# Kernel tuning notes

Hardware: AMD Instinct MI355X
Metric: run time of the kernel (lower is better)

## Reference

```python
import jax, jax.numpy as jnp
import numpy as np

S, B, H = 2048, 2, 2048
NP = 16            # num attention heads
HN = H // NP       # head dim = 128


def setup_inputs() -> dict:
    key = jax.random.key(0)
    k0, k1, k2 = jax.random.split(key, 3)
    hidden_states = jax.random.normal(k0, (S, B, H), dtype=jnp.float32) * 0.02
    w_qkv = jax.random.normal(k1, (3 * H, H), dtype=jnp.float32) * 0.02
    b_qkv = jnp.zeros((3 * H,), dtype=jnp.float32)
    w_dense = jax.random.normal(k2, (H, H), dtype=jnp.float32) * 0.02
    b_dense = jnp.zeros((H,), dtype=jnp.float32)
    # causal mask: True means "mask out" (strictly upper triangular)
    attention_mask = jnp.triu(jnp.ones((S, S), dtype=bool), k=1)[None, None]  # [1,1,S,S]
    return {
        "hidden_states": hidden_states,
        "attention_mask": attention_mask,
        "w_qkv": w_qkv,
        "b_qkv": b_qkv,
        "w_dense": w_dense,
        "b_dense": b_dense,
    }


def reference(hidden_states, attention_mask, w_qkv, b_qkv, w_dense, b_dense):
    s, b, h = hidden_states.shape
    # fused QKV projection (ColumnParallelLinear: y = x @ W^T + b)
    mixed = hidden_states @ w_qkv.T + b_qkv                 # [s,b,3h]
    mixed = mixed.reshape(s, b, NP, 3 * HN)
    q, k, v = jnp.split(mixed, 3, axis=-1)                  # each [s,b,np,hn]
    norm = 1.0 / jnp.sqrt(jnp.asarray(HN, hidden_states.dtype))
    # scaled QK^T -> [b,np,sq,sk]
    scores = jnp.einsum("sbnh,tbnh->bnst", q, k) * norm
    # attention_mask_func: masked_fill(mask, -10000.0)
    scores = jnp.where(attention_mask, jnp.asarray(-10000.0, scores.dtype), scores)
    # softmax in fp32 (softmax_in_fp32)
    probs = jax.nn.softmax(scores.astype(jnp.float32), axis=-1).astype(scores.dtype)
    # AV matmul -> [s,b,np,hn] -> [s,b,h]
    context = jnp.einsum("bnst,tbnh->sbnh", probs, v).reshape(s, b, h)
    # output projection (RowParallelLinear)
    out = context @ w_dense.T + b_dense
    return out
```

## Files before the change

### kernel.cpp

```cpp
#include <hip/hip_runtime.h>
#include <hip/hip_bf16.h>
#include <cstdint>
#include <cstddef>

#define SS   2048
#define BB   2
#define HH   2048
#define NHEAD 16
#define HDIM 128
#define H3   6144
#define MROWS 4096

typedef __attribute__((ext_vector_type(4))) float f32x4;
typedef __attribute__((ext_vector_type(8))) __bf16 bf16x8;
typedef __attribute__((ext_vector_type(8))) unsigned short us8;
typedef __attribute__((ext_vector_type(4))) unsigned short us4;

__device__ __forceinline__ unsigned short f2b(float f) {
    union { float f; unsigned u; } v; v.f = f;
    unsigned r = v.u + 0x7fffu + ((v.u >> 16) & 1u);
    return (unsigned short)(r >> 16);
}

__device__ __forceinline__ bf16x8 ld_b16x8(const unsigned short* p) {
    us8 u = *(const us8*)p;
    return __builtin_bit_cast(bf16x8, u);
}

__device__ __forceinline__ bf16x8 ld8_off(const unsigned short* base, int byteoff) {
    return __builtin_bit_cast(bf16x8, *(const us8*)((const char*)base + byteoff));
}

__device__ __forceinline__ int sw256(int b) { return b ^ (((b >> 8) & 7) << 4); }
__device__ __forceinline__ int sw128(int b) { return b ^ (((b >> 7) & 7) << 4); }

__device__ __forceinline__ void gload_lds16(const unsigned short* g, unsigned short* l) {
    __builtin_amdgcn_global_load_lds(
        (const __attribute__((address_space(1))) unsigned int*)g,
        (__attribute__((address_space(3))) unsigned int*)l, 16, 0, 0);
}

__global__ __launch_bounds__(256) void cvt_f32_bf16(
    const float* __restrict__ in, unsigned short* __restrict__ out, int n4)
{
    const int stride = gridDim.x * blockDim.x;
    for (int i = blockIdx.x * blockDim.x + threadIdx.x; i < n4; i += stride) {
        const float4 v = ((const float4*)in)[i];
        us4 o = { f2b(v.x), f2b(v.y), f2b(v.z), f2b(v.w) };
        ((us4*)out)[i] = o;
    }
}

__global__ __launch_bounds__(256) void transpose_v(
    const unsigned short* __restrict__ mixed,
    unsigned short* __restrict__ vt)
{
    const int st = blockIdx.x;
    const int nh = blockIdx.y;
    const int bb = blockIdx.z;
    const int tid = threadIdx.x;
    __shared__ unsigned short T[64][136];
#pragma unroll
    for (int i = 0; i < 4; ++i) {
        const int c = i * 256 + tid;
        const int sl = c >> 4, d0 = (c & 15) << 3;
        const us8 v = *(const us8*)(mixed +
            ((size_t)(st * 64 + sl) * BB + bb) * H3 + nh * 384 + 256 + d0);
        *(us8*)(&T[sl][d0]) = v;
    }
    __syncthreads();
#pragma unroll
    for (int i = 0; i < 4; ++i) {
        const int c = i * 256 + tid;
        const int d = c >> 3, sl0 = (c & 7) << 3;
        us8 o;
#pragma unroll
        for (int j = 0; j < 8; ++j) o[j] = T[sl0 + j][d];
        *(us8*)(vt + ((size_t)(bb * NHEAD + nh) * HDIM + d) * SS + st * 64 + sl0) = o;
    }
}

#define STAGE_HALF(gp, lo)                                        \
    gload_lds16((gp) + soff[0], smem + (lo) + tid * 8);           \
    gload_lds16((gp) + soff[1], smem + (lo) + 4096 + tid * 8);

template <bool F32OUT>
__global__ __launch_bounds__(512, 2) void gemm_8ph(
    const unsigned short* __restrict__ A,
    const unsigned short* __restrict__ Bw,
    const float* __restrict__ bias,
    void* __restrict__ Cout,
    int Nv, int Kv)
{
    extern __shared__ unsigned short smem[];

    const int tid  = threadIdx.x;
    const int lane = tid & 63;
    const int wave = tid >> 6;
    const int wm = wave >> 2, wn = wave & 3;
    const int bm = blockIdx.y, bn = blockIdx.x;

    const unsigned short* Ab = A  + (size_t)bm * 256 * Kv;
    const unsigned short* Bb = Bw + (size_t)bn * 256 * Kv;

    int soff[2];
#pragma unroll
    for (int i = 0; i < 2; ++i) {
        const int p = (i * 512 + tid) * 16;
        const int l = p ^ (((p >> 7) & 7) << 4);
        soff[i] = (l >> 7) * Kv + ((l & 127) >> 1);
    }

    f32x4 acc[8][4];
#pragma unroll
    for (int m = 0; m < 8; ++m)
#pragma unroll
        for (int n = 0; n < 4; ++n) acc[m][n] = (f32x4){0.f, 0.f, 0.f, 0.f};

    const int frow = lane & 15;
    const int g16  = (lane >> 4) << 4;
    const int swx  = (frow & 7) << 4;
    const int kx0  = g16 ^ swx;
    const int kx1  = (64 + g16) ^ swx;
    const int aRowB = (wm * 128 + frow) * 128;
    const int bRowB = 65536 + (wn * 64 + frow) * 128;

    const int NT = Kv >> 6;

    STAGE_HALF(Ab,                 0);
    STAGE_HALF(Ab + 128 * Kv,      8192);
    STAGE_HALF(Bb,                 32768);
    STAGE_HALF(Bb + 128 * Kv,      40960);
    STAGE_HALF(Bb + 64,            16384 + 32768);
    STAGE_HALF(Bb + 128 * Kv + 64, 16384 + 40960);
    asm volatile("s_waitcnt vmcnt(4)" ::: "memory");
    __builtin_amdgcn_s_barrier();

    for (int t = 0; t < NT; ++t) {
        const int j   = t & 1;
        const int jo  = j * 32768;
        const int joE = j * 16384;
        const int jnE = (j ^ 1) * 16384;
        const int cA  = (t + 1 < NT) ? (t + 1) * 64 : (NT - 1) * 64;
        const int cB  = (t + 2 < NT) ? (t + 2) * 64 : (NT - 1) * 64;

        bf16x8 bb[4][2];

        {
            bf16x8 a00 = ld8_off(smem, jo + aRowB + 0 * 2048 + kx0);
            bf16x8 a01 = ld8_off(smem, jo + aRowB + 0 * 2048 + kx1);
            bf16x8 a10 = ld8_off(smem, jo + aRowB + 1 * 2048 + kx0);
            bf16x8 a11 = ld8_off(smem, jo + aRowB + 1 * 2048 + kx1);
#pragma unroll
            for (int n = 0; n < 4; ++n) {
                bb[n][0] = ld8_off(smem, jo + bRowB + n * 2048 + kx0);
                bb[n][1] = ld8_off(smem, jo + bRowB + n * 2048 + kx1);
            }
            STAGE_HALF(Ab + cA, jnE);
            __builtin_amdgcn_s_barrier();
            asm volatile("s_waitcnt lgkmcnt(0)" ::: "memory");
            __builtin_amdgcn_sched_barrier(0);
            __builtin_amdgcn_s_setprio(1);
#pragma unroll
            for (int n = 0; n < 4; ++n) {
                acc[0][n] = __builtin_amdgcn_mfma_f32_16x16x32_bf16(a00, bb[n][0], acc[0][n], 0, 0, 0);
                acc[0][n] = __builtin_amdgcn_mfma_f32_16x16x32_bf16(a01, bb[n][1], acc[0][n], 0, 0, 0);
                acc[1][n] = __builtin_amdgcn_mfma_f32_16x16x32_bf16(a10, bb[n][0], acc[1][n], 0, 0, 0);
                acc[1][n] = __builtin_amdgcn_mfma_f32_16x16x32_bf16(a11, bb[n][1], acc[1][n], 0, 0, 0);
            }
            __builtin_amdgcn_s_setprio(0);
            __builtin_amdgcn_s_barrier();
        }
        {
            bf16x8 a00 = ld8_off(smem, jo + aRowB + 2 * 2048 + kx0);
            bf16x8 a01 = ld8_off(smem, jo + aRowB + 2 * 2048 + kx1);
            bf16x8 a10 = ld8_off(smem, jo + aRowB + 3 * 2048 + kx0);
            bf16x8 a11 = ld8_off(smem, jo + aRowB + 3 * 2048 + kx1);
            STAGE_HALF(Ab + 128 * Kv + cA, jnE + 8192);
            __builtin_amdgcn_s_barrier();
            asm volatile("s_waitcnt lgkmcnt(0)" ::: "memory");
            __builtin_amdgcn_sched_barrier(0);
            __builtin_amdgcn_s_setprio(1);
#pragma unroll
            for (int n = 0; n < 4; ++n) {
                acc[2][n] = __builtin_amdgcn_mfma_f32_16x16x32_bf16(a00, bb[n][0], acc[2][n], 0, 0, 0);
                acc[2][n] = __builtin_amdgcn_mfma_f32_16x16x32_bf16(a01, bb[n][1], acc[2][n], 0, 0, 0);
                acc[3][n] = __builtin_amdgcn_mfma_f32_16x16x32_bf16(a10, bb[n][0], acc[3][n], 0, 0, 0);
                acc[3][n] = __builtin_amdgcn_mfma_f32_16x16x32_bf16(a11, bb[n][1], acc[3][n], 0, 0, 0);
            }
            __builtin_amdgcn_s_setprio(0);
            __builtin_amdgcn_s_barrier();
        }
        {
            bf16x8 a00 = ld8_off(smem, jo + aRowB + 4 * 2048 + kx0);
            bf16x8 a01 = ld8_off(smem, jo + aRowB + 4 * 2048 + kx1);
            bf16x8 a10 = ld8_off(smem, jo + aRowB + 5 * 2048 + kx0);
            bf16x8 a11 = ld8_off(smem, jo + aRowB + 5 * 2048 + kx1);
            STAGE_HALF(Bb + cB, 32768 + joE);
            __builtin_amdgcn_s_barrier();
            asm volatile("s_waitcnt lgkmcnt(0)" ::: "memory");
            __builtin_amdgcn_sched_barrier(0);
            __builtin_amdgcn_s_setprio(1);
#pragma unroll
            for (int n = 0; n < 4; ++n) {
                acc[4][n] = __builtin_amdgcn_mfma_f32_16x16x32_bf16(a00, bb[n][0], acc[4][n], 0, 0, 0);
                acc[4][n] = __builtin_amdgcn_mfma_f32_16x16x32_bf16(a01, bb[n][1], acc[4][n], 0, 0, 0);
                acc[5][n] = __builtin_amdgcn_mfma_f32_16x16x32_bf16(a10, bb[n][0], acc[5][n], 0, 0, 0);
                acc[5][n] = __builtin_amdgcn_mfma_f32_16x16x32_bf16(a11, bb[n][1], acc[5][n], 0, 0, 0);
            }
            __builtin_amdgcn_s_setprio(0);
            __builtin_amdgcn_s_barrier();
        }
        {
            bf16x8 a00 = ld8_off(smem, jo + aRowB + 6 * 2048 + kx0);
            bf16x8 a01 = ld8_off(smem, jo + aRowB + 6 * 2048 + kx1);
            bf16x8 a10 = ld8_off(smem, jo + aRowB + 7 * 2048 + kx0);
            bf16x8 a11 = ld8_off(smem, jo + aRowB + 7 * 2048 + kx1);
            STAGE_HALF(Bb + 128 * Kv + cB, 32768 + joE + 8192);
            __builtin_amdgcn_s_barrier();
            asm volatile("s_waitcnt lgkmcnt(0)" ::: "memory");
            __builtin_amdgcn_sched_barrier(0);
            __builtin_amdgcn_s_setprio(1);
#pragma unroll
            for (int n = 0; n < 4; ++n) {
                acc[6][n] = __builtin_amdgcn_mfma_f32_16x16x32_bf16(a00, bb[n][0], acc[6][n], 0, 0, 0);
                acc[6][n] = __builtin_amdgcn_mfma_f32_16x16x32_bf16(a01, bb[n][1], acc[6][n], 0, 0, 0);
                acc[7][n] = __builtin_amdgcn_mfma_f32_16x16x32_bf16(a10, bb[n][0], acc[7][n], 0, 0, 0);
                acc[7][n] = __builtin_amdgcn_mfma_f32_16x16x32_bf16(a11, bb[n][1], acc[7][n], 0, 0, 0);
            }
            __builtin_amdgcn_s_setprio(0);
            asm volatile("s_waitcnt vmcnt(4)" ::: "memory");
            __builtin_amdgcn_s_barrier();
        }
    }

    const int r0 = (lane >> 4) << 2;
#pragma unroll
    for (int m = 0; m < 8; ++m) {
        const int row = bm * 256 + wm * 128 + m * 16 + r0;
#pragma unroll
        for (int n = 0; n < 4; ++n) {
            const int col = bn * 256 + wn * 64 + n * 16 + frow;
            const float bv = bias[col];
#pragma unroll
            for (int r = 0; r < 4; ++r) {
                const float o = acc[m][n][r] + bv;
                if (F32OUT) ((float*)Cout)[(size_t)(row + r) * Nv + col] = o;
                else        ((unsigned short*)Cout)[(size_t)(row + r) * Nv + col] = f2b(o);
            }
        }
    }
}

template <bool F32OUT>
__global__ __launch_bounds__(256) void gemm_lds(
    const unsigned short* __restrict__ A,
    const unsigned short* __restrict__ Bw,
    const float* __restrict__ bias,
    void* __restrict__ Cout,
    int Nv, int Kv)
{
    __shared__ unsigned short Ash[128 * 64];
    __shared__ unsigned short Bsh[128 * 64];

    const int tid  = threadIdx.x;
    const int lane = tid & 63;
    const int wave = tid >> 6;
    const int wm = wave >> 1, wn = wave & 1;
    const int bm = blockIdx.y, bn = blockIdx.x;

    const unsigned short* Ab = A  + (size_t)bm * 128 * Kv;
    const unsigned short* Bb = Bw + (size_t)bn * 128 * Kv;

    int srcoff[4];
#pragma unroll
    for (int i = 0; i < 4; ++i) {
        const int p0 = (i * 256 + tid) * 16;
        const int l0 = p0 ^ (((p0 >> 7) & 7) << 4);
        srcoff[i] = (l0 >> 7) * Kv + ((l0 & 127) >> 1);
    }

    f32x4 acc[4][4];
#pragma unroll
    for (int m = 0; m < 4; ++m)
#pragma unroll
        for (int n = 0; n < 4; ++n) acc[m][n] = (f32x4){0.f, 0.f, 0.f, 0.f};

    const int frow = lane & 15;
    const int g16  = (lane >> 4) << 4;
    const int swx  = (frow & 7) << 4;

    for (int kt = 0; kt < Kv; kt += 64) {
#pragma unroll
        for (int i = 0; i < 4; ++i) {
            gload_lds16(Ab + srcoff[i] + kt, Ash + (i * 2048 + wave * 512));
            gload_lds16(Bb + srcoff[i] + kt, Bsh + (i * 2048 + wave * 512));
        }
        __syncthreads();

#pragma unroll
        for (int ks = 0; ks < 2; ++ks) {
            bf16x8 af[4], bfr[4];
#pragma unroll
            for (int m = 0; m < 4; ++m)
                af[m] = ld8_off(Ash, (((wm * 64 + m * 16 + frow) << 7) + ks * 64 + g16) ^ swx);
#pragma unroll
            for (int n = 0; n < 4; ++n)
                bfr[n] = ld8_off(Bsh, (((wn * 64 + n * 16 + frow) << 7) + ks * 64 + g16) ^ swx);
#pragma unroll
            for (int m = 0; m < 4; ++m)
#pragma unroll
                for (int n = 0; n < 4; ++n)
                    acc[m][n] = __builtin_amdgcn_mfma_f32_16x16x32_bf16(af[m], bfr[n], acc[m][n], 0, 0, 0);
        }
        __syncthreads();
    }

    const int r0 = (lane >> 4) << 2;
#pragma unroll
    for (int m = 0; m < 4; ++m) {
        const int row = bm * 128 + wm * 64 + m * 16 + r0;
#pragma unroll
        for (int n = 0; n < 4; ++n) {
            const int col = bn * 128 + wn * 64 + n * 16 + frow;
            const float bv = bias[col];
#pragma unroll
            for (int r = 0; r < 4; ++r) {
                const float o = acc[m][n][r] + bv;
                if (F32OUT) ((float*)Cout)[(size_t)(row + r) * Nv + col] = o;
                else        ((unsigned short*)Cout)[(size_t)(row + r) * Nv + col] = f2b(o);
            }
        }
    }
}

__global__ __launch_bounds__(256) void attn_kernel(
    const unsigned short* __restrict__ mixed,
    const unsigned short* __restrict__ vt,
    unsigned short* __restrict__ context)
{
    const int pair = blockIdx.x;
    const int nh   = blockIdx.y;
    const int bb   = blockIdx.z;
    const int tid  = threadIdx.x;
    const int lane = tid & 63;
    const int wave = tid >> 6;

    __shared__ __align__(1024) unsigned short smem[16384 + 16384 + 4096];

    const int frow = lane & 15;
    const int g16  = (lane >> 4) << 4;
    const int r0   = (lane >> 4) << 2;

    int koff[4], voff[4];
#pragma unroll
    for (int i = 0; i < 4; ++i) {
        const int p0 = (i * 256 + tid) * 16;
        const int lK = p0 ^ (((p0 >> 8) & 7) << 4);
        koff[i] = (lK >> 8) * (BB * H3) + ((lK & 255) >> 1);
        const int lV = p0 ^ (((p0 >> 7) & 7) << 4);
        voff[i] = (lV >> 7) * SS + ((lV & 127) >> 1);
    }

    const unsigned short* kg = mixed + (size_t)bb * H3 + nh * 384 + 128;
    const unsigned short* vg = vt + (size_t)(bb * NHEAD + nh) * HDIM * SS;

    const float norm = 0.088388347648318447f;
    char* Pb = (char*)(smem + 32768) + wave * 2048;

    for (int half = 0; half < 2; ++half) {
        const int qt = half ? (31 - pair) : pair;
        const int q0 = qt * 64 + wave * 16;

        bf16x8 qf[4];
        {
            const unsigned short* qptr =
                mixed + ((size_t)(q0 + frow) * BB + bb) * H3 + nh * 384;
#pragma unroll
            for (int kk = 0; kk < 4; ++kk)
                qf[kk] = ld_b16x8(qptr + kk * 32 + ((lane >> 4) << 3));
        }

        f32x4 Oacc[8];
#pragma unroll
        for (int ct = 0; ct < 8; ++ct) Oacc[ct] = (f32x4){0.f, 0.f, 0.f, 0.f};
        float m_r[4] = {-1e30f, -1e30f, -1e30f, -1e30f};
        float l_r[4] = {0.f, 0.f, 0.f, 0.f};

        {
            unsigned short* Kd = smem + wave * 512;
            unsigned short* Vd = smem + 16384 + wave * 512;
#pragma unroll
            for (int i = 0; i < 4; ++i) {
                gload_lds16(kg + koff[i], Kd + i * 2048);
                gload_lds16(vg + voff[i], Vd + i * 2048);
            }
        }
        __syncthreads();

        int cur = 0;
        for (int kt = 0; kt <= qt; ++kt) {
            if (kt < qt) {
                const unsigned short* kt_g = kg + (size_t)(kt + 1) * 64 * (BB * H3);
                const unsigned short* vt_g = vg + (kt + 1) * 64;
                unsigned short* Kd = smem + (cur ^ 1) * 8192 + wave * 512;
                unsigned short* Vd = smem + 16384 + (cur ^ 1) * 8192 + wave * 512;
#pragma unroll
                for (int i = 0; i < 4; ++i) {
                    gload_lds16(kt_g + koff[i], Kd + i * 2048);
                    gload_lds16(vt_g + voff[i], Vd + i * 2048);
                }
            }

            const unsigned short* Ks = smem + cur * 8192;
            const unsigned short* Vs = smem + 16384 + cur * 8192;
            const int krow0 = kt * 64;

            f32x4 sc4[4];
#pragma unroll
            for (int t = 0; t < 4; ++t) {
                f32x4 s = (f32x4){0.f, 0.f, 0.f, 0.f};
#pragma unroll
                for (int kk = 0; kk < 4; ++kk) {
                    bf16x8 kf = ld8_off(Ks, sw256((t * 16 + frow) * 256 + kk * 64 + g16));
                    s = __builtin_amdgcn_mfma_f32_16x16x32_bf16(qf[kk], kf, s, 0, 0, 0);
                }
                sc4[t] = s;
            }

#pragma unroll
            for (int t = 0; t < 4; ++t) {
                const int kcol = krow0 + t * 16 + frow;
#pragma unroll
                for (int r = 0; r < 4; ++r) {
                    float sv = sc4[t][r] * norm;
                    if (kcol > q0 + r0 + r) sv = -1e30f;
                    sc4[t][r] = sv;
                }
            }

            float tmax[4];
#pragma unroll
            for (int r = 0; r < 4; ++r)
                tmax[r] = fmaxf(fmaxf(sc4[0][r], sc4[1][r]), fmaxf(sc4[2][r], sc4[3][r]));
#pragma unroll
            for (int r = 0; r < 4; ++r) {
                tmax[r] = fmaxf(tmax[r], __shfl_xor(tmax[r], 1, 64));
                tmax[r] = fmaxf(tmax[r], __shfl_xor(tmax[r], 2, 64));
                tmax[r] = fmaxf(tmax[r], __shfl_xor(tmax[r], 4, 64));
                tmax[r] = fmaxf(tmax[r], __shfl_xor(tmax[r], 8, 64));
            }

            float a_r[4], rsum[4];
#pragma unroll
            for (int r = 0; r < 4; ++r) {
                const float mnew = fmaxf(m_r[r], tmax[r]);
                a_r[r] = __expf(m_r[r] - mnew);
                m_r[r] = mnew;
                rsum[r] = 0.f;
            }
#pragma unroll
            for (int t = 0; t < 4; ++t)
#pragma unroll
                for (int r = 0; r < 4; ++r) {
                    const float p = __expf(sc4[t][r] - m_r[r]);
                    sc4[t][r] = p;
                    rsum[r] += p;
                }
#pragma unroll
            for (int r = 0; r < 4; ++r) {
                rsum[r] += __shfl_xor(rsum[r], 1, 64);
                rsum[r] += __shfl_xor(rsum[r], 2, 64);
                rsum[r] += __shfl_xor(rsum[r], 4, 64);
                rsum[r] += __shfl_xor(rsum[r], 8, 64);
                l_r[r] = l_r[r] * a_r[r] + rsum[r];
            }
#pragma unroll
            for (int ct = 0; ct < 8; ++ct)
#pragma unroll
                for (int r = 0; r < 4; ++r) Oacc[ct][r] *= a_r[r];

#pragma unroll
            for (int t = 0; t < 4; ++t)
#pragma unroll
                for (int r = 0; r < 4; ++r)
                    *(unsigned short*)(Pb + sw128((r0 + r) * 128 + (t * 16 + frow) * 2)) =
                        f2b(sc4[t][r]);

#pragma unroll
            for (int ks = 0; ks < 2; ++ks) {
                bf16x8 pf = ld8_off((const unsigned short*)Pb, sw128(frow * 128 + ks * 64 + g16));
#pragma unroll
                for (int ct = 0; ct < 8; ++ct) {
                    bf16x8 vf = ld8_off(Vs, sw128((ct * 16 + frow) * 128 + ks * 64 + g16));
                    Oacc[ct] = __builtin_amdgcn_mfma_f32_16x16x32_bf16(pf, vf, Oacc[ct], 0, 0, 0);
                }
            }

            __syncthreads();
            cur ^= 1;
        }

#pragma unroll
        for (int ct = 0; ct < 8; ++ct) {
            const int d = ct * 16 + frow;
#pragma unroll
            for (int r = 0; r < 4; ++r) {
                const float o = Oacc[ct][r] / l_r[r];
                const size_t row = (size_t)(q0 + r0 + r) * BB + bb;
                context[row * HH + nh * 128 + d] = f2b(o);
            }
        }
    }
}

extern "C" void kernel_launch(void* const* d_in, const int* in_sizes, int n_in,
                              void* d_out, int out_size, void* d_ws, size_t ws_size,
                              hipStream_t stream) {
    const float* hidden  = (const float*)d_in[0];
    const float* w_qkv   = (const float*)d_in[2];
    const float* b_qkv   = (const float*)d_in[3];
    const float* w_dense = (const float*)d_in[4];
    const float* b_dense = (const float*)d_in[5];
    float* out = (float*)d_out;

    unsigned short* mixed = (unsigned short*)d_ws;
    unsigned short* hb    = mixed + (size_t)MROWS * H3;
    unsigned short* wq    = hb + (size_t)MROWS * HH;
    unsigned short* wd    = wq + (size_t)H3 * HH;
    unsigned short* context = hb;
    unsigned short* vtg     = wq;

    dim3 blk(256);
    cvt_f32_bf16<<<2048, blk, 0, stream>>>(hidden, hb, (MROWS * HH) / 4);
    cvt_f32_bf16<<<2048, blk, 0, stream>>>(w_qkv, wq, (H3 * HH) / 4);
    cvt_f32_bf16<<<1024, blk, 0, stream>>>(w_dense, wd, (HH * HH) / 4);

    hipFuncSetAttribute(reinterpret_cast<const void*>(gemm_8ph<false>),
                        hipFuncAttributeMaxDynamicSharedMemorySize, 131072);
    gemm_8ph<false><<<dim3(H3 / 256, MROWS / 256), dim3(512), 131072, stream>>>(
        hb, wq, b_qkv, mixed, H3, HH);
    transpose_v<<<dim3(32, NHEAD, BB), blk, 0, stream>>>(mixed, vtg);
    attn_kernel<<<dim3(16, NHEAD, BB), blk, 0, stream>>>(mixed, vtg, context);
    gemm_lds<true><<<dim3(16, 32), blk, 0, stream>>>(context, wd, b_dense, out, HH, HH);
}
```

Before: 286.5 us.

## Retile QKV GEMM to 128x384 blocks with templated B width

Changes the QKV projection GEMM tile from 256x256 to 128xBN (BN=384). The grid grows from 24x16=384 blocks to 16x32=512 blocks to even out the load across CUs. The LDS staging and the per-phase MFMA schedule are restructured: four phases of one A fragment row against 6 B fragments each, with three B units staged per K-step. A smaller M tile raises global traffic per FLOP for the A operand. The 131072-byte dynamic LDS request is kept although usage appears smaller, which may still limit occupancy.

```diff
diff --git a/kernel.cpp b/kernel.cpp
--- a/kernel.cpp
+++ b/kernel.cpp
@@ -80,11 +80,11 @@
     }
 }
 
-#define STAGE_HALF(gp, lo)                                        \
+#define STAGE_UNIT(gp, lo)                                        \
     gload_lds16((gp) + soff[0], smem + (lo) + tid * 8);           \
     gload_lds16((gp) + soff[1], smem + (lo) + 4096 + tid * 8);
 
-template <bool F32OUT>
+template <int BN, bool F32OUT>
 __global__ __launch_bounds__(512, 2) void gemm_8ph(
     const unsigned short* __restrict__ A,
     const unsigned short* __restrict__ Bw,
@@ -93,6 +93,9 @@
     int Nv, int Kv)
 {
     extern __shared__ unsigned short smem[];
+    constexpr int NF     = BN / 64;
+    constexpr int BUNITS = BN / 128;
+    constexpr int BELEMS = BN * 64;
 
     const int tid  = threadIdx.x;
     const int lane = tid & 63;
@@ -100,8 +103,8 @@
     const int wm = wave >> 2, wn = wave & 3;
     const int bm = blockIdx.y, bn = blockIdx.x;
 
-    const unsigned short* Ab = A  + (size_t)bm * 256 * Kv;
-    const unsigned short* Bb = Bw + (size_t)bn * 256 * Kv;
+    const unsigned short* Ab = A  + (size_t)bm * 128 * Kv;
+    const unsigned short* Bb = Bw + (size_t)bn * BN * Kv;
 
     int soff[2];
 #pragma unroll
@@ -111,136 +114,125 @@
         soff[i] = (l >> 7) * Kv + ((l & 127) >> 1);
     }
 
-    f32x4 acc[8][4];
-#pragma unroll
-    for (int m = 0; m < 8; ++m)
-#pragma unroll
-        for (int n = 0; n < 4; ++n) acc[m][n] = (f32x4){0.f, 0.f, 0.f, 0.f};
+    f32x4 acc[4][NF];
+#pragma unroll
+    for (int m = 0; m < 4; ++m)
+#pragma unroll
+        for (int n = 0; n < NF; ++n) acc[m][n] = (f32x4){0.f, 0.f, 0.f, 0.f};
 
     const int frow = lane & 15;
     const int g16  = (lane >> 4) << 4;
     const int swx  = (frow & 7) << 4;
     const int kx0  = g16 ^ swx;
     const int kx1  = (64 + g16) ^ swx;
-    const int aRowB = (wm * 128 + frow) * 128;
-    const int bRowB = 65536 + (wn * 64 + frow) * 128;
+    const int aRow = (wm * 64 + frow) * 128;
+    const int bRow = 32768 + (wn * (BN / 4) + frow) * 128;
 
     const int NT = Kv >> 6;
 
-    STAGE_HALF(Ab,                 0);
-    STAGE_HALF(Ab + 128 * Kv,      8192);
-    STAGE_HALF(Bb,                 32768);
-    STAGE_HALF(Bb + 128 * Kv,      40960);
-    STAGE_HALF(Bb + 64,            16384 + 32768);
-    STAGE_HALF(Bb + 128 * Kv + 64, 16384 + 40960);
-    asm volatile("s_waitcnt vmcnt(4)" ::: "memory");
+    STAGE_UNIT(Ab, 0);
+    STAGE_UNIT(Bb, 16384);
+    STAGE_UNIT(Bb + 128 * Kv, 16384 + 8192);
+    if constexpr (BUNITS == 3) { STAGE_UNIT(Bb + 256 * Kv, 16384 + 16384); }
+    STAGE_UNIT(Bb + 64, 16384 + BELEMS);
+    STAGE_UNIT(Bb + 128 * Kv + 64, 16384 + BELEMS + 8192);
+    if constexpr (BUNITS == 3) { STAGE_UNIT(Bb + 256 * Kv + 64, 16384 + BELEMS + 16384); }
+    if constexpr (BUNITS == 3) { asm volatile("s_waitcnt vmcnt(6)" ::: "memory"); }
+    else                       { asm volatile("s_waitcnt vmcnt(4)" ::: "memory"); }
     __builtin_amdgcn_s_barrier();
 
     for (int t = 0; t < NT; ++t) {
-        const int j   = t & 1;
-        const int jo  = j * 32768;
-        const int joE = j * 16384;
-        const int jnE = (j ^ 1) * 16384;
-        const int cA  = (t + 1 < NT) ? (t + 1) * 64 : (NT - 1) * 64;
-        const int cB  = (t + 2 < NT) ? (t + 2) * 64 : (NT - 1) * 64;
-
-        bf16x8 bb[4][2];
+        const int j  = t & 1;
+        const int jn = j ^ 1;
+        const int aj = j * 16384;
+        const int bj = j * (BN * 128);
+        const int cA = ((t + 1 < NT) ? (t + 1) : (NT - 1)) * 64;
+        const int cB = ((t + 2 < NT) ? (t + 2) : (NT - 1)) * 64;
+
+        bf16x8 bbf[NF][2];
 
         {
-            bf16x8 a00 = ld8_off(smem, jo + aRowB + 0 * 2048 + kx0);
-            bf16x8 a01 = ld8_off(smem, jo + aRowB + 0 * 2048 + kx1);
-            bf16x8 a10 = ld8_off(smem, jo + aRowB + 1 * 2048 + kx0);
-            bf16x8 a11 = ld8_off(smem, jo + aRowB + 1 * 2048 + kx1);
-#pragma unroll
-            for (int n = 0; n < 4; ++n) {
-                bb[n][0] = ld8_off(smem, jo + bRowB + n * 2048 + kx0);
-                bb[n][1] = ld8_off(smem, jo + bRowB + n * 2048 + kx1);
-            }
-            STAGE_HALF(Ab + cA, jnE);
+            bf16x8 a0 = ld8_off(smem, aj + aRow + 0 * 2048 + kx0);
+            bf16x8 a1 = ld8_off(smem, aj + aRow + 0 * 2048 + kx1);
+#pragma unroll
+            for (int n = 0; n < NF; ++n) {
+                bbf[n][0] = ld8_off(smem, bj + bRow + n * 2048 + kx0);
+                bbf[n][1] = ld8_off(smem, bj + bRow + n * 2048 + kx1);
+            }
+            STAGE_UNIT(Ab + cA, jn * 8192);
             __builtin_amdgcn_s_barrier();
             asm volatile("s_waitcnt lgkmcnt(0)" ::: "memory");
             __builtin_amdgcn_sched_barrier(0);
             __builtin_amdgcn_s_setprio(1);
 #pragma unroll
-            for (int n = 0; n < 4; ++n) {
-                acc[0][n] = __builtin_amdgcn_mfma_f32_16x16x32_bf16(a00, bb[n][0], acc[0][n], 0, 0, 0);
-                acc[0][n] = __builtin_amdgcn_mfma_f32_16x16x32_bf16(a01, bb[n][1], acc[0][n], 0, 0, 0);
-                acc[1][n] = __builtin_amdgcn_mfma_f32_16x16x32_bf16(a10, bb[n][0], acc[1][n], 0, 0, 0);
-                acc[1][n] = __builtin_amdgcn_mfma_f32_16x16x32_bf16(a11, bb[n][1], acc[1][n], 0, 0, 0);
+            for (int n = 0; n < NF; ++n) {
+                acc[0][n] = __builtin_amdgcn_mfma_f32_16x16x32_bf16(a0, bbf[n][0], acc[0][n], 0, 0, 0);
+                acc[0][n] = __builtin_amdgcn_mfma_f32_16x16x32_bf16(a1, bbf[n][1], acc[0][n], 0, 0, 0);
             }
             __builtin_amdgcn_s_setprio(0);
             __builtin_amdgcn_s_barrier();
         }
         {
-            bf16x8 a00 = ld8_off(smem, jo + aRowB + 2 * 2048 + kx0);
-            bf16x8 a01 = ld8_off(smem, jo + aRowB + 2 * 2048 + kx1);
-            bf16x8 a10 = ld8_off(smem, jo + aRowB + 3 * 2048 + kx0);
-            bf16x8 a11 = ld8_off(smem, jo + aRowB + 3 * 2048 + kx1);
-            STAGE_HALF(Ab + 128 * Kv + cA, jnE + 8192);
+            bf16x8 a0 = ld8_off(smem, aj + aRow + 1 * 2048 + kx0);
+            bf16x8 a1 = ld8_off(smem, aj + aRow + 1 * 2048 + kx1);
+            STAGE_UNIT(Bb + cB, 16384 + j * BELEMS);
             __builtin_amdgcn_s_barrier();
             asm volatile("s_waitcnt lgkmcnt(0)" ::: "memory");
             __builtin_amdgcn_sched_barrier(0);
             __builtin_amdgcn_s_setprio(1);
 #pragma unroll
-            for (int n = 0; n < 4; ++n) {
-                acc[2][n] = __builtin_amdgcn_mfma_f32_16x16x32_bf16(a00, bb[n][0], acc[2][n], 0, 0, 0);
-                acc[2][n] = __builtin_amdgcn_mfma_f32_16x16x32_bf16(a01, bb[n][1], acc[2][n], 0, 0, 0);
-                acc[3][n] = __builtin_amdgcn_mfma_f32_16x16x32_bf16(a10, bb[n][0], acc[3][n], 0, 0, 0);
-                acc[3][n] = __builtin_amdgcn_mfma_f32_16x16x32_bf16(a11, bb[n][1], acc[3][n], 0, 0, 0);
+            for (int n = 0; n < NF; ++n) {
+                acc[1][n] = __builtin_amdgcn_mfma_f32_16x16x32_bf16(a0, bbf[n][0], acc[1][n], 0, 0, 0);
+                acc[1][n] = __builtin_amdgcn_mfma_f32_16x16x32_bf16(a1, bbf[n][1], acc[1][n], 0, 0, 0);
             }
             __builtin_amdgcn_s_setprio(0);
             __builtin_amdgcn_s_barrier();
         }
         {
-            bf16x8 a00 = ld8_off(smem, jo + aRowB + 4 * 2048 + kx0);
-            bf16x8 a01 = ld8_off(smem, jo + aRowB + 4 * 2048 + kx1);
-            bf16x8 a10 = ld8_off(smem, jo + aRowB + 5 * 2048 + kx0);
-            bf16x8 a11 = ld8_off(smem, jo + aRowB + 5 * 2048 + kx1);
-            STAGE_HALF(Bb + cB, 32768 + joE);
+            bf16x8 a0 = ld8_off(smem, aj + aRow + 2 * 2048 + kx0);
+            bf16x8 a1 = ld8_off(smem, aj + aRow + 2 * 2048 + kx1);
+            STAGE_UNIT(Bb + 128 * Kv + cB, 16384 + j * BELEMS + 8192);
             __builtin_amdgcn_s_barrier();
             asm volatile("s_waitcnt lgkmcnt(0)" ::: "memory");
             __builtin_amdgcn_sched_barrier(0);
             __builtin_amdgcn_s_setprio(1);
 #pragma unroll
-            for (int n = 0; n < 4; ++n) {
-                acc[4][n] = __builtin_amdgcn_mfma_f32_16x16x32_bf16(a00, bb[n][0], acc[4][n], 0, 0, 0);
-                acc[4][n] = __builtin_amdgcn_mfma_f32_16x16x32_bf16(a01, bb[n][1], acc[4][n], 0, 0, 0);
-                acc[5][n] = __builtin_amdgcn_mfma_f32_16x16x32_bf16(a10, bb[n][0], acc[5][n], 0, 0, 0);
-                acc[5][n] = __builtin_amdgcn_mfma_f32_16x16x32_bf16(a11, bb[n][1], acc[5][n], 0, 0, 0);
+            for (int n = 0; n < NF; ++n) {
+                acc[2][n] = __builtin_amdgcn_mfma_f32_16x16x32_bf16(a0, bbf[n][0], acc[2][n], 0, 0, 0);
+                acc[2][n] = __builtin_amdgcn_mfma_f32_16x16x32_bf16(a1, bbf[n][1], acc[2][n], 0, 0, 0);
             }
             __builtin_amdgcn_s_setprio(0);
             __builtin_amdgcn_s_barrier();
         }
         {
-            bf16x8 a00 = ld8_off(smem, jo + aRowB + 6 * 2048 + kx0);
-            bf16x8 a01 = ld8_off(smem, jo + aRowB + 6 * 2048 + kx1);
-            bf16x8 a10 = ld8_off(smem, jo + aRowB + 7 * 2048 + kx0);
-            bf16x8 a11 = ld8_off(smem, jo + aRowB + 7 * 2048 + kx1);
-            STAGE_HALF(Bb + 128 * Kv + cB, 32768 + joE + 8192);
+            bf16x8 a0 = ld8_off(smem, aj + aRow + 3 * 2048 + kx0);
+            bf16x8 a1 = ld8_off(smem, aj + aRow + 3 * 2048 + kx1);
+            if constexpr (BUNITS == 3) {
+                STAGE_UNIT(Bb + 256 * Kv + cB, 16384 + j * BELEMS + 16384);
+            }
             __builtin_amdgcn_s_barrier();
             asm volatile("s_waitcnt lgkmcnt(0)" ::: "memory");
             __builtin_amdgcn_sched_barrier(0);
             __builtin_amdgcn_s_setprio(1);
 #pragma unroll
-            for (int n = 0; n < 4; ++n) {
-                acc[6][n] = __builtin_amdgcn_mfma_f32_16x16x32_bf16(a00, bb[n][0], acc[6][n], 0, 0, 0);
-                acc[6][n] = __builtin_amdgcn_mfma_f32_16x16x32_bf16(a01, bb[n][1], acc[6][n], 0, 0, 0);
-                acc[7][n] = __builtin_amdgcn_mfma_f32_16x16x32_bf16(a10, bb[n][0], acc[7][n], 0, 0, 0);
-                acc[7][n] = __builtin_amdgcn_mfma_f32_16x16x32_bf16(a11, bb[n][1], acc[7][n], 0, 0, 0);
+            for (int n = 0; n < NF; ++n) {
+                acc[3][n] = __builtin_amdgcn_mfma_f32_16x16x32_bf16(a0, bbf[n][0], acc[3][n], 0, 0, 0);
+                acc[3][n] = __builtin_amdgcn_mfma_f32_16x16x32_bf16(a1, bbf[n][1], acc[3][n], 0, 0, 0);
             }
             __builtin_amdgcn_s_setprio(0);
-            asm volatile("s_waitcnt vmcnt(4)" ::: "memory");
+            if constexpr (BUNITS == 3) { asm volatile("s_waitcnt vmcnt(6)" ::: "memory"); }
+            else                       { asm volatile("s_waitcnt vmcnt(4)" ::: "memory"); }
             __builtin_amdgcn_s_barrier();
         }
     }
 
     const int r0 = (lane >> 4) << 2;
 #pragma unroll
-    for (int m = 0; m < 8; ++m) {
-        const int row = bm * 256 + wm * 128 + m * 16 + r0;
-#pragma unroll
-        for (int n = 0; n < 4; ++n) {
-            const int col = bn * 256 + wn * 64 + n * 16 + frow;
+    for (int m = 0; m < 4; ++m) {
+        const int row = bm * 128 + wm * 64 + m * 16 + r0;
+#pragma unroll
+        for (int n = 0; n < NF; ++n) {
+            const int col = bn * BN + wn * (BN / 4) + n * 16 + frow;
             const float bv = bias[col];
 #pragma unroll
             for (int r = 0; r < 4; ++r) {
@@ -536,9 +528,9 @@
     cvt_f32_bf16<<<2048, blk, 0, stream>>>(w_qkv, wq, (H3 * HH) / 4);
     cvt_f32_bf16<<<1024, blk, 0, stream>>>(w_dense, wd, (HH * HH) / 4);
 
-    hipFuncSetAttribute(reinterpret_cast<const void*>(gemm_8ph<false>),
+    hipFuncSetAttribute(reinterpret_cast<const void*>(gemm_8ph<384, false>),
                         hipFuncAttributeMaxDynamicSharedMemorySize, 131072);
-    gemm_8ph<false><<<dim3(H3 / 256, MROWS / 256), dim3(512), 131072, stream>>>(
+    gemm_8ph<384, false><<<dim3(H3 / 384, MROWS / 128), dim3(512), 131072, stream>>>(
         hb, wq, b_qkv, mixed, H3, HH);
     transpose_v<<<dim3(32, NHEAD, BB), blk, 0, stream>>>(mixed, vtg);
     attn_kernel<<<dim3(16, NHEAD, BB), blk, 0, stream>>>(mixed, vtg, context);
```

After: 279.0 us. -2.6%, faster.
